# Kernel tuning notes

Hardware: AMD Instinct MI355X
Metric: run time of the kernel (lower is better)

## Reference

```python
import jax, jax.numpy as jnp
import numpy as np

N = 100000        # total nodes (60000 type-0 + 40000 type-1)
E = 1600000       # edges (avg degree 16)
D = 128           # num_hidden
C = 16            # num_classes


def _glorot(key, fan_in, fan_out):
    # xavier_normal with gain 1.414 (as in the torch module inits)
    std = 1.414 * (2.0 / (fan_in + fan_out)) ** 0.5
    return jax.random.normal(key, (fan_in, fan_out), jnp.float32) * std


def setup_inputs() -> dict:
    key = jax.random.key(0)
    ks = jax.random.split(key, 12)
    feat0 = jax.random.normal(ks[0], (60000, 512), jnp.float32)
    feat1 = jax.random.normal(ks[1], (40000, 256), jnp.float32)
    src = jax.random.randint(ks[2], (E,), 0, N, jnp.int32)
    dst = jax.random.randint(ks[3], (E,), 0, N, jnp.int32)
    return {
        "feat0": feat0,
        "feat1": feat1,
        "src": src,
        "dst": dst,
        "W_fc0": _glorot(ks[4], 512, D), "b_fc0": jnp.zeros((D,), jnp.float32),
        "W_fc1": _glorot(ks[5], 256, D), "b_fc1": jnp.zeros((D,), jnp.float32),
        "W_g0": _glorot(ks[6], D, D),   "b_g0": jnp.zeros((D,), jnp.float32),
        "W_g1": _glorot(ks[7], D, D),   "b_g1": jnp.zeros((D,), jnp.float32),
        "W_out": _glorot(ks[8], D, C),  "b_out": jnp.zeros((C,), jnp.float32),
    }


def reference(feat0, feat1, src, dst,
              W_fc0, b_fc0, W_fc1, b_fc1,
              W_g0, b_g0, W_g1, b_g1, W_out, b_out):
    # per-type input projections, then concat over node types -> (N, D)
    h = jnp.concatenate([feat0 @ W_fc0 + b_fc0, feat1 @ W_fc1 + b_fc1], axis=0)

    # in-degree for 'mean' reduce (DGL mean yields 0 for isolated nodes; clamp avoids /0)
    deg = jax.ops.segment_sum(jnp.ones((E,), jnp.float32), dst, num_segments=N)
    inv_deg = (1.0 / jnp.maximum(deg, 1.0))[:, None]

    def gin(h, W, b):
        # copy_u + mean reduce: neigh[i] = mean_{(j->i) in E} h[j]
        neigh = jax.ops.segment_sum(h[src], dst, num_segments=N) * inv_deg
        # (1 + eps) * h + neigh with eps = 0, then apply_func (Linear), then sigmoid
        return jax.nn.sigmoid((h + neigh) @ W + b)

    h = gin(h, W_g0, b_g0)      # gat_layers[0]
    h = gin(h, W_g1, b_g1)      # gat_layers[1]
    logits = gin(h, W_out, b_out)  # gat_layers[-1] -> (N, C)
    # logits.unsqueeze(1).mean(1) is a no-op
    return logits
```

## Files before the change

### kernel.cpp

```cpp
#include <hip/hip_runtime.h>
#include <hip/hip_bf16.h>

#define N_NODES 100000
#define N0_ROWS 60000
#define N1_ROWS 40000
#define NE 1600000
#define HD 128
#define NB 782
#define BSH 128
#define EPB 2560
#define NBLK 625

typedef __attribute__((ext_vector_type(8))) short short8;
typedef __attribute__((ext_vector_type(4))) float f32x4;

__device__ __forceinline__ float bf16lo(unsigned v) { return __uint_as_float(v << 16); }
__device__ __forceinline__ float bf16hi(unsigned v) { return __uint_as_float(v & 0xFFFF0000u); }

__device__ __forceinline__ unsigned short f2bf_rne(float f) {
    unsigned u = __float_as_uint(f);
    return (unsigned short)((u + 0x7FFFu + ((u >> 16) & 1u)) >> 16);
}
__device__ __forceinline__ unsigned pack2_rne(float lo, float hi) {
    unsigned a = __float_as_uint(lo); a = (a + 0x7FFFu + ((a >> 16) & 1u)) >> 16;
    unsigned b = __float_as_uint(hi); b = (b + 0x7FFFu + ((b >> 16) & 1u)) & 0xFFFF0000u;
    return (a & 0xFFFFu) | b;
}
__device__ __forceinline__ float sigmoidf_(float v) { return 1.0f / (1.0f + __expf(-v)); }

__global__ __launch_bounds__(256) void k_phist(const int* __restrict__ dst,
                                               int* __restrict__ cnt) {
    __shared__ int h[NB];
    int blk = blockIdx.x;
    for (int i = threadIdx.x; i < NB; i += 256) h[i] = 0;
    __syncthreads();
    int e0 = blk * EPB;
    for (int e = e0 + threadIdx.x; e < e0 + EPB; e += 256)
        atomicAdd(&h[dst[e] >> 7], 1);
    __syncthreads();
    for (int i = threadIdx.x; i < NB; i += 256)
        cnt[i * NBLK + blk] = h[i];
}

__global__ __launch_bounds__(64) void k_colscan(int* __restrict__ cnt,
                                                int* __restrict__ bcnt) {
    int b = blockIdx.x, lane = threadIdx.x & 63;
    int* col = cnt + (size_t)b * NBLK;
    int carry = 0;
    for (int base = 0; base < NBLK; base += 64) {
        int i = base + lane;
        int v = (i < NBLK) ? col[i] : 0;
        int s = v;
        #pragma unroll
        for (int off = 1; off < 64; off <<= 1) {
            int t = __shfl_up(s, off);
            if (lane >= off) s += t;
        }
        if (i < NBLK) col[i] = carry + s - v;
        carry += __shfl(s, 63);
    }
    if (lane == 0) bcnt[b] = carry;
}

__global__ void k_bscan(const int* __restrict__ bcnt, int* __restrict__ boff,
                        int* __restrict__ rowptr) {
    int lane = threadIdx.x & 63;
    const int CH = (NB + 63) / 64;
    int base = lane * CH;
    int t = 0;
    for (int c = 0; c < CH; ++c) {
        int i = base + c;
        t += (i < NB) ? bcnt[i] : 0;
    }
    int s = t;
    #pragma unroll
    for (int off = 1; off < 64; off <<= 1) {
        int u = __shfl_up(s, off);
        if (lane >= off) s += u;
    }
    int running = s - t;
    for (int c = 0; c < CH; ++c) {
        int i = base + c;
        if (i < NB) {
            boff[i] = running;
            running += bcnt[i];
        }
    }
    if (lane == 0) { boff[NB] = NE; rowptr[N_NODES] = NE; }
}

__global__ __launch_bounds__(256) void k_pplace(const int* __restrict__ src,
                                                const int* __restrict__ dst,
                                                const int* __restrict__ boff,
                                                const int* __restrict__ cnt,
                                                unsigned* __restrict__ ebuf) {
    __shared__ int h[NB];
    int blk = blockIdx.x;
    for (int i = threadIdx.x; i < NB; i += 256) h[i] = cnt[i * NBLK + blk];
    __syncthreads();
    int e0 = blk * EPB;
    for (int e = e0 + threadIdx.x; e < e0 + EPB; e += 256) {
        int d = dst[e];
        int b = d >> 7;
        int pos = atomicAdd(&h[b], 1);
        ebuf[boff[b] + pos] = ((unsigned)(d & 127) << 17) | (unsigned)src[e];
    }
}

__global__ __launch_bounds__(256) void k_bplace(const unsigned* __restrict__ ebuf,
                                                const int* __restrict__ boff,
                                                int* __restrict__ rowptr,
                                                float* __restrict__ invd,
                                                int* __restrict__ eidx) {
    __shared__ int cnt[BSH], off[BSH], lcnt[BSH];
    int b = blockIdx.x, tid = threadIdx.x;
    int e0 = boff[b], e1 = boff[b + 1];
    for (int i = tid; i < BSH; i += 256) { cnt[i] = 0; lcnt[i] = 0; }
    __syncthreads();
    for (int e = e0 + tid; e < e1; e += 256)
        atomicAdd(&cnt[ebuf[e] >> 17], 1);
    __syncthreads();
    if (tid < 64) {
        int lane = tid;
        int c0 = cnt[2 * lane], c1 = cnt[2 * lane + 1];
        int t = c0 + c1, s = t;
        #pragma unroll
        for (int o = 1; o < 64; o <<= 1) {
            int u = __shfl_up(s, o);
            if (lane >= o) s += u;
        }
        int excl = s - t;
        off[2 * lane] = excl;
        off[2 * lane + 1] = excl + c0;
    }
    __syncthreads();
    for (int i = tid; i < BSH; i += 256) {
        int node = b * BSH + i;
        if (node < N_NODES) {
            rowptr[node] = e0 + off[i];
            invd[node] = 1.0f / fmaxf((float)cnt[i], 1.0f);
        }
    }
    for (int e = e0 + tid; e < e1; e += 256) {
        unsigned ent = ebuf[e];
        int d = ent >> 17;
        int pos = e0 + off[d] + atomicAdd(&lcnt[d], 1);
        eidx[pos] = (int)(ent & 0x1FFFFu);
    }
}

__global__ void prep_w_all(const float* __restrict__ W0, unsigned short* __restrict__ T0,
                           const float* __restrict__ W1, unsigned short* __restrict__ T1,
                           const float* __restrict__ W2, unsigned short* __restrict__ T2,
                           const float* __restrict__ W3, unsigned short* __restrict__ T3,
                           const float* __restrict__ W4, unsigned short* __restrict__ T4) {
    int gid = blockIdx.x * blockDim.x + threadIdx.x;
    int stride = gridDim.x * blockDim.x;
    const int S0 = 512 * 128, S1 = 256 * 128, S2 = 128 * 128, S3 = 128 * 128, S4 = 128 * 16;
    const int E1 = S0 + S1, E2 = E1 + S2, E3 = E2 + S3, E4 = E3 + S4;
    for (int i = gid; i < E4; i += stride) {
        if (i < S0) {
            int n = i / 512, k = i - n * 512;
            T0[i] = f2bf_rne(W0[k * 128 + n]);
        } else if (i < E1) {
            int j = i - S0; int n = j / 256, k = j - n * 256;
            T1[j] = f2bf_rne(W1[k * 128 + n]);
        } else if (i < E2) {
            int j = i - E1; int n = j / 128, k = j - n * 128;
            T2[j] = f2bf_rne(W2[k * 128 + n]);
        } else if (i < E3) {
            int j = i - E2; int n = j / 128, k = j - n * 128;
            T3[j] = f2bf_rne(W3[k * 128 + n]);
        } else {
            int j = i - E3; int n = j / 128, k = j - n * 128;
            T4[j] = f2bf_rne(W4[k * 16 + n]);
        }
    }
}

template <int K>
__global__ __launch_bounds__(512, 4) void k_proj(const float* __restrict__ feat,
                                                 const unsigned short* __restrict__ Wt,
                                                 const float* __restrict__ bias,
                                                 unsigned short* __restrict__ hout,
                                                 int ntiles, int row_off) {
    constexpr int KC = K / 32;
    __shared__ unsigned short A_lds[16][K + 8];

    const int tid = threadIdx.x;
    const int lane = tid & 63, w = tid >> 6;
    const int g = lane >> 4, r16 = lane & 15;
    const int col = w * 16 + r16;

    short8 fb[KC];
    #pragma unroll
    for (int kc = 0; kc < KC; ++kc)
        fb[kc] = *reinterpret_cast<const short8*>(Wt + (size_t)col * K + kc * 32 + g * 8);
    const float bv = bias[col];

    const int srow = tid >> 5;
    const int sseg = tid & 31;

    for (int tile = blockIdx.x; tile < ntiles; tile += gridDim.x) {
        __syncthreads();
        const float4* rowp = reinterpret_cast<const float4*>(feat + (size_t)(tile * 16 + srow) * K);
        #pragma unroll
        for (int s = 0; s < K / 128; ++s) {
            float4 v = rowp[sseg + s * 32];
            unsigned lo = __builtin_amdgcn_perm(__float_as_uint(v.y), __float_as_uint(v.x), 0x07060302u);
            unsigned hi = __builtin_amdgcn_perm(__float_as_uint(v.w), __float_as_uint(v.z), 0x07060302u);
            *reinterpret_cast<uint2*>(&A_lds[srow][(sseg + s * 32) * 4]) = make_uint2(lo, hi);
        }
        __syncthreads();
        f32x4 acc = {0.f, 0.f, 0.f, 0.f};
        #pragma unroll
        for (int kc = 0; kc < KC; ++kc) {
            short8 fa = *reinterpret_cast<const short8*>(&A_lds[r16][kc * 32 + g * 8]);
            acc = __builtin_amdgcn_mfma_f32_16x16x32_bf16(fa, fb[kc], acc, 0, 0, 0);
        }
        #pragma unroll
        for (int r = 0; r < 4; ++r) {
            size_t orow = (size_t)(row_off + tile * 16 + g * 4 + r);
            hout[orow * HD + col] = f2bf_rne(acc[r] + bv);
        }
    }
}

__global__ __launch_bounds__(256, 4) void k_z_gemm(const unsigned short* __restrict__ x,
                                                   const unsigned short* __restrict__ Wt,
                                                   unsigned short* __restrict__ zout) {
    const int lane = threadIdx.x & 63, wid = threadIdx.x >> 6;
    const int g = lane >> 4, r16 = lane & 15;
    const int colbase = wid * 32;

    short8 fb[2][4];
    #pragma unroll
    for (int nt = 0; nt < 2; ++nt) {
        int n = colbase + nt * 16 + r16;
        #pragma unroll
        for (int kc = 0; kc < 4; ++kc)
            fb[nt][kc] = *reinterpret_cast<const short8*>(Wt + (size_t)n * HD + kc * 32 + g * 8);
    }

    const int ntiles = N_NODES / 16;
    for (int tile = blockIdx.x; tile < ntiles; tile += gridDim.x) {
        const unsigned short* ap = x + (size_t)(tile * 16 + r16) * HD;
        f32x4 acc0 = {0.f, 0.f, 0.f, 0.f};
        f32x4 acc1 = {0.f, 0.f, 0.f, 0.f};
        #pragma unroll
        for (int kc = 0; kc < 4; ++kc) {
            short8 fa = *reinterpret_cast<const short8*>(ap + kc * 32 + g * 8);
            acc0 = __builtin_amdgcn_mfma_f32_16x16x32_bf16(fa, fb[0][kc], acc0, 0, 0, 0);
            acc1 = __builtin_amdgcn_mfma_f32_16x16x32_bf16(fa, fb[1][kc], acc1, 0, 0, 0);
        }
        #pragma unroll
        for (int r = 0; r < 4; ++r) {
            size_t orow = (size_t)(tile * 16 + g * 4 + r);
            zout[orow * HD + colbase + r16]      = f2bf_rne(acc0[r]);
            zout[orow * HD + colbase + 16 + r16] = f2bf_rne(acc1[r]);
        }
    }
}

__global__ __launch_bounds__(256, 4) void k_aggz(const unsigned short* __restrict__ z,
                                                 const int* __restrict__ rowptr,
                                                 const int* __restrict__ eidx,
                                                 const float* __restrict__ invd,
                                                 const float* __restrict__ bias,
                                                 unsigned short* __restrict__ hout) {
    const unsigned* zp = reinterpret_cast<const unsigned*>(z);
    unsigned* hp = reinterpret_cast<unsigned*>(hout);
    int lane = threadIdx.x & 63, wid = threadIdx.x >> 6;
    float blo = bias[2 * lane], bhi = bias[2 * lane + 1];
    int nwaves = gridDim.x * 4;
    for (int node = blockIdx.x * 4 + wid; node < N_NODES; node += nwaves) {
        int rp0 = rowptr[node], rp1 = rowptr[node + 1];
        float a0 = 0.f, a1 = 0.f;
        for (int base = rp0; base < rp1; base += 64) {
            int m = rp1 - base; if (m > 64) m = 64;
            int idx = (lane < m) ? eidx[base + lane] : 0;
            int t = 0;
            for (; t + 4 <= m; t += 4) {
                int j0 = __shfl(idx, t), j1 = __shfl(idx, t + 1);
                int j2 = __shfl(idx, t + 2), j3 = __shfl(idx, t + 3);
                unsigned v0 = zp[(size_t)j0 * 64 + lane];
                unsigned v1 = zp[(size_t)j1 * 64 + lane];
                unsigned v2 = zp[(size_t)j2 * 64 + lane];
                unsigned v3 = zp[(size_t)j3 * 64 + lane];
                a0 += bf16lo(v0) + bf16lo(v1) + bf16lo(v2) + bf16lo(v3);
                a1 += bf16hi(v0) + bf16hi(v1) + bf16hi(v2) + bf16hi(v3);
            }
            for (; t < m; ++t) {
                int j = __shfl(idx, t);
                unsigned v = zp[(size_t)j * 64 + lane];
                a0 += bf16lo(v); a1 += bf16hi(v);
            }
        }
        unsigned zv = zp[(size_t)node * 64 + lane];
        float s = invd[node];
        hp[(size_t)node * 64 + lane] = pack2_rne(sigmoidf_(bf16lo(zv) + s * a0 + blo),
                                                 sigmoidf_(bf16hi(zv) + s * a1 + bhi));
    }
}

__global__ __launch_bounds__(256, 4) void k_zout_gemm(const unsigned short* __restrict__ x,
                                                      const unsigned short* __restrict__ Wt,
                                                      unsigned short* __restrict__ z3) {
    const int lane = threadIdx.x & 63, wid = threadIdx.x >> 6;
    const int g = lane >> 4, r16 = lane & 15;

    short8 fb[4];
    #pragma unroll
    for (int kc = 0; kc < 4; ++kc)
        fb[kc] = *reinterpret_cast<const short8*>(Wt + (size_t)r16 * HD + kc * 32 + g * 8);

    const int ntiles = N_NODES / 16;
    for (int tile = blockIdx.x * 4 + wid; tile < ntiles; tile += gridDim.x * 4) {
        const unsigned short* ap = x + (size_t)(tile * 16 + r16) * HD;
        f32x4 acc = {0.f, 0.f, 0.f, 0.f};
        #pragma unroll
        for (int kc = 0; kc < 4; ++kc) {
            short8 fa = *reinterpret_cast<const short8*>(ap + kc * 32 + g * 8);
            acc = __builtin_amdgcn_mfma_f32_16x16x32_bf16(fa, fb[kc], acc, 0, 0, 0);
        }
        #pragma unroll
        for (int r = 0; r < 4; ++r)
            z3[(size_t)(tile * 16 + g * 4 + r) * 16 + r16] = f2bf_rne(acc[r]);
    }
}

__global__ __launch_bounds__(256, 4) void k_agg16(const unsigned short* __restrict__ z3,
                                                  const int* __restrict__ rowptr,
                                                  const int* __restrict__ eidx,
                                                  const float* __restrict__ invd,
                                                  const float* __restrict__ bias,
                                                  float* __restrict__ out) {
    const unsigned* zp = reinterpret_cast<const unsigned*>(z3);
    int lane = threadIdx.x & 63, wid = threadIdx.x >> 6;
    int grp = lane >> 3, sub = lane & 7;
    float blo = bias[2 * sub], bhi = bias[2 * sub + 1];
    int step = gridDim.x * 32;
    for (int nb = blockIdx.x * 32 + wid * 8; nb < N_NODES; nb += step) {
        int node = nb + grp;
        bool valid = node < N_NODES;
        int rp0 = valid ? rowptr[node] : 0;
        int rp1 = valid ? rowptr[node + 1] : 0;
        float a0 = 0.f, a1 = 0.f;
        for (int base = rp0; base < rp1; base += 8) {
            int m = rp1 - base; if (m > 8) m = 8;
            int idx = (sub < m) ? eidx[base + sub] : 0;
            #pragma unroll
            for (int t = 0; t < 8; ++t) {
                if (t < m) {
                    int j = __shfl(idx, (grp << 3) + t);
                    unsigned v = zp[(size_t)j * 8 + sub];
                    a0 += bf16lo(v); a1 += bf16hi(v);
                }
            }
        }
        if (valid) {
            unsigned zv = zp[(size_t)node * 8 + sub];
            float s = invd[node];
            out[(size_t)node * 16 + sub * 2]     = sigmoidf_(bf16lo(zv) + s * a0 + blo);
            out[(size_t)node * 16 + sub * 2 + 1] = sigmoidf_(bf16hi(zv) + s * a1 + bhi);
        }
    }
}

extern "C" void kernel_launch(void* const* d_in, const int* in_sizes, int n_in,
                              void* d_out, int out_size, void* d_ws, size_t ws_size,
                              hipStream_t stream) {
    const float* feat0 = (const float*)d_in[0];
    const float* feat1 = (const float*)d_in[1];
    const int*   src   = (const int*)d_in[2];
    const int*   dst   = (const int*)d_in[3];
    const float* Wfc0  = (const float*)d_in[4];
    const float* bfc0  = (const float*)d_in[5];
    const float* Wfc1  = (const float*)d_in[6];
    const float* bfc1  = (const float*)d_in[7];
    const float* Wg0   = (const float*)d_in[8];
    const float* bg0   = (const float*)d_in[9];
    const float* Wg1   = (const float*)d_in[10];
    const float* bg1   = (const float*)d_in[11];
    const float* Wout  = (const float*)d_in[12];
    const float* bout  = (const float*)d_in[13];

    char* w = (char*)d_ws;
    auto alloc = [&](size_t bytes) {
        char* p = w;
        w += (bytes + 255) & ~(size_t)255;
        return p;
    };
    unsigned short* h      = (unsigned short*)alloc((size_t)N_NODES * HD * 2);
    unsigned short* z      = (unsigned short*)alloc((size_t)N_NODES * HD * 2);
    unsigned short* z3     = (unsigned short*)alloc((size_t)N_NODES * 16 * 2);
    int*   rowptr = (int*)alloc((size_t)(N_NODES + 1) * 4);
    float* invd   = (float*)alloc((size_t)N_NODES * 4);
    int*   eidx   = (int*)alloc((size_t)NE * 4);
    int*   cnt    = (int*)alloc((size_t)NB * NBLK * 4);
    int*   bcnt   = (int*)alloc((size_t)NB * 4);
    int*   boff   = (int*)alloc((size_t)(NB + 1) * 4);
    unsigned short* Wt_fc0 = (unsigned short*)alloc(512 * 128 * 2);
    unsigned short* Wt_fc1 = (unsigned short*)alloc(256 * 128 * 2);
    unsigned short* Wt_g0  = (unsigned short*)alloc(128 * 128 * 2);
    unsigned short* Wt_g1  = (unsigned short*)alloc(128 * 128 * 2);
    unsigned short* Wt_out = (unsigned short*)alloc(128 * 16 * 2);
    unsigned* ebuf = (unsigned*)z;

    k_phist<<<NBLK, 256, 0, stream>>>(dst, cnt);
    k_colscan<<<NB, 64, 0, stream>>>(cnt, bcnt);
    k_bscan<<<1, 64, 0, stream>>>(bcnt, boff, rowptr);
    k_pplace<<<NBLK, 256, 0, stream>>>(src, dst, boff, cnt, ebuf);
    k_bplace<<<NB, 256, 0, stream>>>(ebuf, boff, rowptr, invd, eidx);

    prep_w_all<<<520, 256, 0, stream>>>(Wfc0, Wt_fc0, Wfc1, Wt_fc1,
                                        Wg0, Wt_g0, Wg1, Wt_g1, Wout, Wt_out);

    k_proj<512><<<512, 512, 0, stream>>>(feat0, Wt_fc0, bfc0, h, N0_ROWS / 16, 0);
    k_proj<256><<<512, 512, 0, stream>>>(feat1, Wt_fc1, bfc1, h, N1_ROWS / 16, N0_ROWS);

    k_z_gemm<<<2084, 256, 0, stream>>>(h, Wt_g0, z);
    k_aggz<<<2048, 256, 0, stream>>>(z, rowptr, eidx, invd, bg0, h);
    k_z_gemm<<<2084, 256, 0, stream>>>(h, Wt_g1, z);
    k_aggz<<<2048, 256, 0, stream>>>(z, rowptr, eidx, invd, bg1, h);
    k_zout_gemm<<<1563, 256, 0, stream>>>(h, Wt_out, z3);
    k_agg16<<<2048, 256, 0, stream>>>(z3, rowptr, eidx, invd, bout, (float*)d_out);
}
```

Baseline: 304.0 us.

## Fuse dense GEMMs into projection and aggregation kernels via LDS tiles

The next layer's 128x128 GEMM now runs inside the input projection kernel, so z = h·W_g0 is produced directly from LDS and h never goes to global memory. Each GIN aggregation is fused with the following GEMM. A block gathers 16 nodes into an LDS tile and then runs the MFMA on that tile, which removes the separate z_gemm and zout_gemm launches and their h round-trips. In exchange, the aggregation is now tied to fixed 16-node tiles with block-wide barriers, so load imbalance across degrees can stall whole blocks, and the 16-class kernel uses only one wave for its MFMA. ebuf now gets its own buffer instead of aliasing z.

```diff
diff --git a/kernel.cpp b/kernel.cpp
--- a/kernel.cpp
+++ b/kernel.cpp
@@ -179,13 +179,15 @@
 }
 
 template <int K>
-__global__ __launch_bounds__(512, 4) void k_proj(const float* __restrict__ feat,
-                                                 const unsigned short* __restrict__ Wt,
-                                                 const float* __restrict__ bias,
-                                                 unsigned short* __restrict__ hout,
-                                                 int ntiles, int row_off) {
+__global__ __launch_bounds__(512, 4) void k_proj_fused(const float* __restrict__ feat,
+                                                       const unsigned short* __restrict__ Wt,
+                                                       const float* __restrict__ bias,
+                                                       const unsigned short* __restrict__ Wg,
+                                                       unsigned short* __restrict__ zout,
+                                                       int ntiles, int row_off) {
     constexpr int KC = K / 32;
     __shared__ unsigned short A_lds[16][K + 8];
+    __shared__ unsigned short h_lds[16][HD + 8];
 
     const int tid = threadIdx.x;
     const int lane = tid & 63, w = tid >> 6;
@@ -196,6 +198,10 @@
     #pragma unroll
     for (int kc = 0; kc < KC; ++kc)
         fb[kc] = *reinterpret_cast<const short8*>(Wt + (size_t)col * K + kc * 32 + g * 8);
+    short8 fbg[4];
+    #pragma unroll
+    for (int kc = 0; kc < 4; ++kc)
+        fbg[kc] = *reinterpret_cast<const short8*>(Wg + (size_t)col * HD + kc * 32 + g * 8);
     const float bv = bias[col];
 
     const int srow = tid >> 5;
@@ -219,16 +225,32 @@
             acc = __builtin_amdgcn_mfma_f32_16x16x32_bf16(fa, fb[kc], acc, 0, 0, 0);
         }
         #pragma unroll
+        for (int r = 0; r < 4; ++r)
+            h_lds[g * 4 + r][col] = f2bf_rne(acc[r] + bv);
+        __syncthreads();
+        f32x4 accz = {0.f, 0.f, 0.f, 0.f};
+        #pragma unroll
+        for (int kc = 0; kc < 4; ++kc) {
+            short8 fa = *reinterpret_cast<const short8*>(&h_lds[r16][kc * 32 + g * 8]);
+            accz = __builtin_amdgcn_mfma_f32_16x16x32_bf16(fa, fbg[kc], accz, 0, 0, 0);
+        }
+        #pragma unroll
         for (int r = 0; r < 4; ++r) {
             size_t orow = (size_t)(row_off + tile * 16 + g * 4 + r);
-            hout[orow * HD + col] = f2bf_rne(acc[r] + bv);
-        }
-    }
-}
-
-__global__ __launch_bounds__(256, 4) void k_z_gemm(const unsigned short* __restrict__ x,
-                                                   const unsigned short* __restrict__ Wt,
-                                                   unsigned short* __restrict__ zout) {
+            zout[orow * HD + col] = f2bf_rne(accz[r]);
+        }
+    }
+}
+
+__global__ __launch_bounds__(256, 4) void k_agg_gemm128(const unsigned short* __restrict__ z,
+                                                        const int* __restrict__ rowptr,
+                                                        const int* __restrict__ eidx,
+                                                        const float* __restrict__ invd,
+                                                        const float* __restrict__ bias,
+                                                        const unsigned short* __restrict__ Wt,
+                                                        unsigned short* __restrict__ zout) {
+    __shared__ unsigned short h_lds[16][HD + 8];
+    const unsigned* zp = reinterpret_cast<const unsigned*>(z);
     const int lane = threadIdx.x & 63, wid = threadIdx.x >> 6;
     const int g = lane >> 4, r16 = lane & 15;
     const int colbase = wid * 32;
@@ -241,15 +263,48 @@
         for (int kc = 0; kc < 4; ++kc)
             fb[nt][kc] = *reinterpret_cast<const short8*>(Wt + (size_t)n * HD + kc * 32 + g * 8);
     }
+    const float blo = bias[2 * lane], bhi = bias[2 * lane + 1];
 
     const int ntiles = N_NODES / 16;
     for (int tile = blockIdx.x; tile < ntiles; tile += gridDim.x) {
-        const unsigned short* ap = x + (size_t)(tile * 16 + r16) * HD;
+        __syncthreads();
+        #pragma unroll
+        for (int q = 0; q < 4; ++q) {
+            int node = tile * 16 + wid * 4 + q;
+            int rp0 = rowptr[node], rp1 = rowptr[node + 1];
+            float a0 = 0.f, a1 = 0.f;
+            for (int base = rp0; base < rp1; base += 64) {
+                int m = rp1 - base; if (m > 64) m = 64;
+                int idx = (lane < m) ? eidx[base + lane] : 0;
+                int t = 0;
+                for (; t + 4 <= m; t += 4) {
+                    int j0 = __shfl(idx, t), j1 = __shfl(idx, t + 1);
+                    int j2 = __shfl(idx, t + 2), j3 = __shfl(idx, t + 3);
+                    unsigned v0 = zp[(size_t)j0 * 64 + lane];
+                    unsigned v1 = zp[(size_t)j1 * 64 + lane];
+                    unsigned v2 = zp[(size_t)j2 * 64 + lane];
+                    unsigned v3 = zp[(size_t)j3 * 64 + lane];
+                    a0 += bf16lo(v0) + bf16lo(v1) + bf16lo(v2) + bf16lo(v3);
+                    a1 += bf16hi(v0) + bf16hi(v1) + bf16hi(v2) + bf16hi(v3);
+                }
+                for (; t < m; ++t) {
+                    int j = __shfl(idx, t);
+                    unsigned v = zp[(size_t)j * 64 + lane];
+                    a0 += bf16lo(v); a1 += bf16hi(v);
+                }
+            }
+            unsigned zv = zp[(size_t)node * 64 + lane];
+            float s = invd[node];
+            *reinterpret_cast<unsigned*>(&h_lds[wid * 4 + q][2 * lane]) =
+                pack2_rne(sigmoidf_(bf16lo(zv) + s * a0 + blo),
+                          sigmoidf_(bf16hi(zv) + s * a1 + bhi));
+        }
+        __syncthreads();
         f32x4 acc0 = {0.f, 0.f, 0.f, 0.f};
         f32x4 acc1 = {0.f, 0.f, 0.f, 0.f};
         #pragma unroll
         for (int kc = 0; kc < 4; ++kc) {
-            short8 fa = *reinterpret_cast<const short8*>(ap + kc * 32 + g * 8);
+            short8 fa = *reinterpret_cast<const short8*>(&h_lds[r16][kc * 32 + g * 8]);
             acc0 = __builtin_amdgcn_mfma_f32_16x16x32_bf16(fa, fb[0][kc], acc0, 0, 0, 0);
             acc1 = __builtin_amdgcn_mfma_f32_16x16x32_bf16(fa, fb[1][kc], acc1, 0, 0, 0);
         }
@@ -262,50 +317,15 @@
     }
 }
 
-__global__ __launch_bounds__(256, 4) void k_aggz(const unsigned short* __restrict__ z,
-                                                 const int* __restrict__ rowptr,
-                                                 const int* __restrict__ eidx,
-                                                 const float* __restrict__ invd,
-                                                 const float* __restrict__ bias,
-                                                 unsigned short* __restrict__ hout) {
+__global__ __launch_bounds__(256, 4) void k_agg_gemm16(const unsigned short* __restrict__ z,
+                                                       const int* __restrict__ rowptr,
+                                                       const int* __restrict__ eidx,
+                                                       const float* __restrict__ invd,
+                                                       const float* __restrict__ bias,
+                                                       const unsigned short* __restrict__ Wt,
+                                                       unsigned short* __restrict__ z3) {
+    __shared__ unsigned short h_lds[16][HD + 8];
     const unsigned* zp = reinterpret_cast<const unsigned*>(z);
-    unsigned* hp = reinterpret_cast<unsigned*>(hout);
-    int lane = threadIdx.x & 63, wid = threadIdx.x >> 6;
-    float blo = bias[2 * lane], bhi = bias[2 * lane + 1];
-    int nwaves = gridDim.x * 4;
-    for (int node = blockIdx.x * 4 + wid; node < N_NODES; node += nwaves) {
-        int rp0 = rowptr[node], rp1 = rowptr[node + 1];
-        float a0 = 0.f, a1 = 0.f;
-        for (int base = rp0; base < rp1; base += 64) {
-            int m = rp1 - base; if (m > 64) m = 64;
-            int idx = (lane < m) ? eidx[base + lane] : 0;
-            int t = 0;
-            for (; t + 4 <= m; t += 4) {
-                int j0 = __shfl(idx, t), j1 = __shfl(idx, t + 1);
-                int j2 = __shfl(idx, t + 2), j3 = __shfl(idx, t + 3);
-                unsigned v0 = zp[(size_t)j0 * 64 + lane];
-                unsigned v1 = zp[(size_t)j1 * 64 + lane];
-                unsigned v2 = zp[(size_t)j2 * 64 + lane];
-                unsigned v3 = zp[(size_t)j3 * 64 + lane];
-                a0 += bf16lo(v0) + bf16lo(v1) + bf16lo(v2) + bf16lo(v3);
-                a1 += bf16hi(v0) + bf16hi(v1) + bf16hi(v2) + bf16hi(v3);
-            }
-            for (; t < m; ++t) {
-                int j = __shfl(idx, t);
-                unsigned v = zp[(size_t)j * 64 + lane];
-                a0 += bf16lo(v); a1 += bf16hi(v);
-            }
-        }
-        unsigned zv = zp[(size_t)node * 64 + lane];
-        float s = invd[node];
-        hp[(size_t)node * 64 + lane] = pack2_rne(sigmoidf_(bf16lo(zv) + s * a0 + blo),
-                                                 sigmoidf_(bf16hi(zv) + s * a1 + bhi));
-    }
-}
-
-__global__ __launch_bounds__(256, 4) void k_zout_gemm(const unsigned short* __restrict__ x,
-                                                      const unsigned short* __restrict__ Wt,
-                                                      unsigned short* __restrict__ z3) {
     const int lane = threadIdx.x & 63, wid = threadIdx.x >> 6;
     const int g = lane >> 4, r16 = lane & 15;
 
@@ -313,19 +333,54 @@
     #pragma unroll
     for (int kc = 0; kc < 4; ++kc)
         fb[kc] = *reinterpret_cast<const short8*>(Wt + (size_t)r16 * HD + kc * 32 + g * 8);
+    const float blo = bias[2 * lane], bhi = bias[2 * lane + 1];
 
     const int ntiles = N_NODES / 16;
-    for (int tile = blockIdx.x * 4 + wid; tile < ntiles; tile += gridDim.x * 4) {
-        const unsigned short* ap = x + (size_t)(tile * 16 + r16) * HD;
-        f32x4 acc = {0.f, 0.f, 0.f, 0.f};
-        #pragma unroll
-        for (int kc = 0; kc < 4; ++kc) {
-            short8 fa = *reinterpret_cast<const short8*>(ap + kc * 32 + g * 8);
-            acc = __builtin_amdgcn_mfma_f32_16x16x32_bf16(fa, fb[kc], acc, 0, 0, 0);
-        }
-        #pragma unroll
-        for (int r = 0; r < 4; ++r)
-            z3[(size_t)(tile * 16 + g * 4 + r) * 16 + r16] = f2bf_rne(acc[r]);
+    for (int tile = blockIdx.x; tile < ntiles; tile += gridDim.x) {
+        __syncthreads();
+        #pragma unroll
+        for (int q = 0; q < 4; ++q) {
+            int node = tile * 16 + wid * 4 + q;
+            int rp0 = rowptr[node], rp1 = rowptr[node + 1];
+            float a0 = 0.f, a1 = 0.f;
+            for (int base = rp0; base < rp1; base += 64) {
+                int m = rp1 - base; if (m > 64) m = 64;
+                int idx = (lane < m) ? eidx[base + lane] : 0;
+                int t = 0;
+                for (; t + 4 <= m; t += 4) {
+                    int j0 = __shfl(idx, t), j1 = __shfl(idx, t + 1);
+                    int j2 = __shfl(idx, t + 2), j3 = __shfl(idx, t + 3);
+                    unsigned v0 = zp[(size_t)j0 * 64 + lane];
+                    unsigned v1 = zp[(size_t)j1 * 64 + lane];
+                    unsigned v2 = zp[(size_t)j2 * 64 + lane];
+                    unsigned v3 = zp[(size_t)j3 * 64 + lane];
+                    a0 += bf16lo(v0) + bf16lo(v1) + bf16lo(v2) + bf16lo(v3);
+                    a1 += bf16hi(v0) + bf16hi(v1) + bf16hi(v2) + bf16hi(v3);
+                }
+                for (; t < m; ++t) {
+                    int j = __shfl(idx, t);
+                    unsigned v = zp[(size_t)j * 64 + lane];
+                    a0 += bf16lo(v); a1 += bf16hi(v);
+                }
+            }
+            unsigned zv = zp[(size_t)node * 64 + lane];
+            float s = invd[node];
+            *reinterpret_cast<unsigned*>(&h_lds[wid * 4 + q][2 * lane]) =
+                pack2_rne(sigmoidf_(bf16lo(zv) + s * a0 + blo),
+                          sigmoidf_(bf16hi(zv) + s * a1 + bhi));
+        }
+        __syncthreads();
+        if (wid == 0) {
+            f32x4 acc = {0.f, 0.f, 0.f, 0.f};
+            #pragma unroll
+            for (int kc = 0; kc < 4; ++kc) {
+                short8 fa = *reinterpret_cast<const short8*>(&h_lds[r16][kc * 32 + g * 8]);
+                acc = __builtin_amdgcn_mfma_f32_16x16x32_bf16(fa, fb[kc], acc, 0, 0, 0);
+            }
+            #pragma unroll
+            for (int r = 0; r < 4; ++r)
+                z3[(size_t)(tile * 16 + g * 4 + r) * 16 + r16] = f2bf_rne(acc[r]);
+        }
     }
 }
 
@@ -391,12 +446,13 @@
         w += (bytes + 255) & ~(size_t)255;
         return p;
     };
-    unsigned short* h      = (unsigned short*)alloc((size_t)N_NODES * HD * 2);
-    unsigned short* z      = (unsigned short*)alloc((size_t)N_NODES * HD * 2);
+    unsigned short* zA     = (unsigned short*)alloc((size_t)N_NODES * HD * 2);
+    unsigned short* zB     = (unsigned short*)alloc((size_t)N_NODES * HD * 2);
     unsigned short* z3     = (unsigned short*)alloc((size_t)N_NODES * 16 * 2);
     int*   rowptr = (int*)alloc((size_t)(N_NODES + 1) * 4);
     float* invd   = (float*)alloc((size_t)N_NODES * 4);
     int*   eidx   = (int*)alloc((size_t)NE * 4);
+    unsigned* ebuf = (unsigned*)alloc((size_t)NE * 4);
     int*   cnt    = (int*)alloc((size_t)NB * NBLK * 4);
     int*   bcnt   = (int*)alloc((size_t)NB * 4);
     int*   boff   = (int*)alloc((size_t)(NB + 1) * 4);
@@ -405,7 +461,6 @@
     unsigned short* Wt_g0  = (unsigned short*)alloc(128 * 128 * 2);
     unsigned short* Wt_g1  = (unsigned short*)alloc(128 * 128 * 2);
     unsigned short* Wt_out = (unsigned short*)alloc(128 * 16 * 2);
-    unsigned* ebuf = (unsigned*)z;
 
     k_phist<<<NBLK, 256, 0, stream>>>(dst, cnt);
     k_colscan<<<NB, 64, 0, stream>>>(cnt, bcnt);
@@ -416,13 +471,10 @@
     prep_w_all<<<520, 256, 0, stream>>>(Wfc0, Wt_fc0, Wfc1, Wt_fc1,
                                         Wg0, Wt_g0, Wg1, Wt_g1, Wout, Wt_out);
 
-    k_proj<512><<<512, 512, 0, stream>>>(feat0, Wt_fc0, bfc0, h, N0_ROWS / 16, 0);
-    k_proj<256><<<512, 512, 0, stream>>>(feat1, Wt_fc1, bfc1, h, N1_ROWS / 16, N0_ROWS);
-
-    k_z_gemm<<<2084, 256, 0, stream>>>(h, Wt_g0, z);
-    k_aggz<<<2048, 256, 0, stream>>>(z, rowptr, eidx, invd, bg0, h);
-    k_z_gemm<<<2084, 256, 0, stream>>>(h, Wt_g1, z);
-    k_aggz<<<2048, 256, 0, stream>>>(z, rowptr, eidx, invd, bg1, h);
-    k_zout_gemm<<<1563, 256, 0, stream>>>(h, Wt_out, z3);
+    k_proj_fused<512><<<512, 512, 0, stream>>>(feat0, Wt_fc0, bfc0, Wt_g0, zA, N0_ROWS / 16, 0);
+    k_proj_fused<256><<<512, 512, 0, stream>>>(feat1, Wt_fc1, bfc1, Wt_g0, zA, N1_ROWS / 16, N0_ROWS);
+
+    k_agg_gemm128<<<2084, 256, 0, stream>>>(zA, rowptr, eidx, invd, bg0, Wt_g1, zB);
+    k_agg_gemm16<<<2084, 256, 0, stream>>>(zB, rowptr, eidx, invd, bg1, Wt_out, z3);
     k_agg16<<<2048, 256, 0, stream>>>(z3, rowptr, eidx, invd, bout, (float*)d_out);
 }
```

Result: slower. 319.1 us (+5.0%).

## Gather neighbours from an FP8 copy of z and fuse projection with first GEMM

Applied to the files above, without the earlier changes.

The input-projection kernel now also runs the first GIN weight GEMM from LDS, so the h tensor is never written out and read back before layer 0. The z GEMMs additionally emit an FP8 (e4m3) packed copy of z. The mean-aggregation kernels gather neighbour rows from that FP8 copy, halving the bytes moved by the random per-edge loads, while keeping the bf16 z for the self term. This trades numerical accuracy in the neighbour sum for reduced gather bandwidth. It also adds extra LDS round trips and barriers in the GEMM kernels, plus a separate edge buffer allocation.

```diff
diff --git a/kernel.cpp b/kernel.cpp
--- a/kernel.cpp
+++ b/kernel.cpp
@@ -13,6 +13,7 @@
 
 typedef __attribute__((ext_vector_type(8))) short short8;
 typedef __attribute__((ext_vector_type(4))) float f32x4;
+typedef __attribute__((ext_vector_type(2))) float f32x2;
 
 __device__ __forceinline__ float bf16lo(unsigned v) { return __uint_as_float(v << 16); }
 __device__ __forceinline__ float bf16hi(unsigned v) { return __uint_as_float(v & 0xFFFF0000u); }
@@ -27,6 +28,56 @@
     return (a & 0xFFFFu) | b;
 }
 __device__ __forceinline__ float sigmoidf_(float v) { return 1.0f / (1.0f + __expf(-v)); }
+
+#if defined(__has_builtin)
+#if __has_builtin(__builtin_amdgcn_cvt_pk_fp8_f32) && __has_builtin(__builtin_amdgcn_cvt_pk_f32_fp8)
+#define HAS_FP8_CVT 1
+#endif
+#endif
+
+#ifdef HAS_FP8_CVT
+__device__ __forceinline__ unsigned pack4_fp8(float c0, float c1, float c2, float c3) {
+    int r = 0;
+    r = __builtin_amdgcn_cvt_pk_fp8_f32(c0, c1, r, false);
+    r = __builtin_amdgcn_cvt_pk_fp8_f32(c2, c3, r, true);
+    return (unsigned)r;
+}
+__device__ __forceinline__ f32x2 unpack2_fp8(unsigned u16) {
+    return __builtin_amdgcn_cvt_pk_f32_fp8((int)u16, false);
+}
+#else
+__device__ __forceinline__ unsigned enc1_fp8(float f) {
+    f = fminf(448.f, fmaxf(-448.f, f));
+    float a = fabsf(f);
+    unsigned s = (__float_as_uint(f) >> 31) << 7;
+    if (a >= 0.015625f) {
+        unsigned u = __float_as_uint(a);
+        u += 0x7FFFFu + ((u >> 20) & 1u);
+        int E = (int)((u >> 23) & 255) - 120;
+        unsigned m3 = (u >> 20) & 7;
+        if (E > 15) { E = 15; m3 = 6; }
+        return s | ((unsigned)E << 3) | m3;
+    } else {
+        int q = (int)rintf(a * 512.f);
+        if (q >= 8) return s | (1u << 3);
+        return s | (unsigned)q;
+    }
+}
+__device__ __forceinline__ unsigned pack4_fp8(float c0, float c1, float c2, float c3) {
+    return enc1_fp8(c0) | (enc1_fp8(c1) << 8) | (enc1_fp8(c2) << 16) | (enc1_fp8(c3) << 24);
+}
+__device__ __forceinline__ float dec1_fp8(unsigned b) {
+    unsigned s = (b >> 7) & 1, e = (b >> 3) & 15, m = b & 7;
+    float v = e ? ldexpf((float)(8 + m), (int)e - 10) : ldexpf((float)m, -9);
+    return s ? -v : v;
+}
+__device__ __forceinline__ f32x2 unpack2_fp8(unsigned u16) {
+    f32x2 r;
+    r[0] = dec1_fp8(u16 & 0xFFu);
+    r[1] = dec1_fp8((u16 >> 8) & 0xFFu);
+    return r;
+}
+#endif
 
 __global__ __launch_bounds__(256) void k_phist(const int* __restrict__ dst,
                                                int* __restrict__ cnt) {
@@ -179,13 +230,16 @@
 }
 
 template <int K>
-__global__ __launch_bounds__(512, 4) void k_proj(const float* __restrict__ feat,
-                                                 const unsigned short* __restrict__ Wt,
-                                                 const float* __restrict__ bias,
-                                                 unsigned short* __restrict__ hout,
-                                                 int ntiles, int row_off) {
+__global__ __launch_bounds__(512, 4) void k_proj_fused(const float* __restrict__ feat,
+                                                       const unsigned short* __restrict__ Wt,
+                                                       const float* __restrict__ bias,
+                                                       const unsigned short* __restrict__ Wg,
+                                                       unsigned short* __restrict__ zout,
+                                                       unsigned* __restrict__ z8out,
+                                                       int ntiles, int row_off) {
     constexpr int KC = K / 32;
     __shared__ unsigned short A_lds[16][K + 8];
+    __shared__ unsigned short h_lds[16][HD + 8];
 
     const int tid = threadIdx.x;
     const int lane = tid & 63, w = tid >> 6;
@@ -196,6 +250,10 @@
     #pragma unroll
     for (int kc = 0; kc < KC; ++kc)
         fb[kc] = *reinterpret_cast<const short8*>(Wt + (size_t)col * K + kc * 32 + g * 8);
+    short8 fbg[4];
+    #pragma unroll
+    for (int kc = 0; kc < 4; ++kc)
+        fbg[kc] = *reinterpret_cast<const short8*>(Wg + (size_t)col * HD + kc * 32 + g * 8);
     const float bv = bias[col];
 
     const int srow = tid >> 5;
@@ -219,19 +277,47 @@
             acc = __builtin_amdgcn_mfma_f32_16x16x32_bf16(fa, fb[kc], acc, 0, 0, 0);
         }
         #pragma unroll
+        for (int r = 0; r < 4; ++r)
+            h_lds[g * 4 + r][col] = f2bf_rne(acc[r] + bv);
+        __syncthreads();
+        f32x4 accz = {0.f, 0.f, 0.f, 0.f};
+        #pragma unroll
+        for (int kc = 0; kc < 4; ++kc) {
+            short8 fa = *reinterpret_cast<const short8*>(&h_lds[r16][kc * 32 + g * 8]);
+            accz = __builtin_amdgcn_mfma_f32_16x16x32_bf16(fa, fbg[kc], accz, 0, 0, 0);
+        }
+        #pragma unroll
         for (int r = 0; r < 4; ++r) {
             size_t orow = (size_t)(row_off + tile * 16 + g * 4 + r);
-            hout[orow * HD + col] = f2bf_rne(acc[r] + bv);
+            zout[orow * HD + col] = f2bf_rne(accz[r]);
+        }
+        __syncthreads();
+        #pragma unroll
+        for (int r = 0; r < 4; ++r)
+            h_lds[g * 4 + r][col] = f2bf_rne(accz[r]);
+        __syncthreads();
+        {
+            int c4 = sseg * 4;
+            unsigned p = pack4_fp8(
+                bf16lo((unsigned)h_lds[srow][c4])     ,
+                bf16lo((unsigned)h_lds[srow][c4 + 1]) ,
+                bf16lo((unsigned)h_lds[srow][c4 + 2]) ,
+                bf16lo((unsigned)h_lds[srow][c4 + 3]) );
+            z8out[(size_t)(row_off + tile * 16 + srow) * 32 + sseg] = p;
         }
     }
 }
 
 __global__ __launch_bounds__(256, 4) void k_z_gemm(const unsigned short* __restrict__ x,
                                                    const unsigned short* __restrict__ Wt,
-                                                   unsigned short* __restrict__ zout) {
+                                                   unsigned short* __restrict__ zout,
+                                                   unsigned* __restrict__ z8out) {
+    __shared__ unsigned short h_lds[16][HD + 8];
     const int lane = threadIdx.x & 63, wid = threadIdx.x >> 6;
     const int g = lane >> 4, r16 = lane & 15;
     const int colbase = wid * 32;
+    const int prow = threadIdx.x >> 4;
+    const int pseg = threadIdx.x & 15;
 
     short8 fb[2][4];
     #pragma unroll
@@ -253,21 +339,43 @@
             acc0 = __builtin_amdgcn_mfma_f32_16x16x32_bf16(fa, fb[0][kc], acc0, 0, 0, 0);
             acc1 = __builtin_amdgcn_mfma_f32_16x16x32_bf16(fa, fb[1][kc], acc1, 0, 0, 0);
         }
+        __syncthreads();
         #pragma unroll
         for (int r = 0; r < 4; ++r) {
             size_t orow = (size_t)(tile * 16 + g * 4 + r);
-            zout[orow * HD + colbase + r16]      = f2bf_rne(acc0[r]);
-            zout[orow * HD + colbase + 16 + r16] = f2bf_rne(acc1[r]);
-        }
-    }
-}
-
-__global__ __launch_bounds__(256, 4) void k_aggz(const unsigned short* __restrict__ z,
-                                                 const int* __restrict__ rowptr,
-                                                 const int* __restrict__ eidx,
-                                                 const float* __restrict__ invd,
-                                                 const float* __restrict__ bias,
-                                                 unsigned short* __restrict__ hout) {
+            unsigned short zb0 = f2bf_rne(acc0[r]);
+            unsigned short zb1 = f2bf_rne(acc1[r]);
+            zout[orow * HD + colbase + r16]      = zb0;
+            zout[orow * HD + colbase + 16 + r16] = zb1;
+            h_lds[g * 4 + r][colbase + r16]      = zb0;
+            h_lds[g * 4 + r][colbase + 16 + r16] = zb1;
+        }
+        __syncthreads();
+        {
+            int c8 = pseg * 8;
+            unsigned p0 = pack4_fp8(
+                bf16lo((unsigned)h_lds[prow][c8])     ,
+                bf16lo((unsigned)h_lds[prow][c8 + 1]) ,
+                bf16lo((unsigned)h_lds[prow][c8 + 2]) ,
+                bf16lo((unsigned)h_lds[prow][c8 + 3]) );
+            unsigned p1 = pack4_fp8(
+                bf16lo((unsigned)h_lds[prow][c8 + 4]) ,
+                bf16lo((unsigned)h_lds[prow][c8 + 5]) ,
+                bf16lo((unsigned)h_lds[prow][c8 + 6]) ,
+                bf16lo((unsigned)h_lds[prow][c8 + 7]) );
+            *reinterpret_cast<uint2*>(&z8out[(size_t)(tile * 16 + prow) * 32 + pseg * 2]) =
+                make_uint2(p0, p1);
+        }
+    }
+}
+
+__global__ __launch_bounds__(256, 4) void k_aggz8(const unsigned short* __restrict__ z,
+                                                  const unsigned short* __restrict__ z8,
+                                                  const int* __restrict__ rowptr,
+                                                  const int* __restrict__ eidx,
+                                                  const float* __restrict__ invd,
+                                                  const float* __restrict__ bias,
+                                                  unsigned short* __restrict__ hout) {
     const unsigned* zp = reinterpret_cast<const unsigned*>(z);
     unsigned* hp = reinterpret_cast<unsigned*>(hout);
     int lane = threadIdx.x & 63, wid = threadIdx.x >> 6;
@@ -275,7 +383,7 @@
     int nwaves = gridDim.x * 4;
     for (int node = blockIdx.x * 4 + wid; node < N_NODES; node += nwaves) {
         int rp0 = rowptr[node], rp1 = rowptr[node + 1];
-        float a0 = 0.f, a1 = 0.f;
+        float a0 = 0.f, a1 = 0.f, b0 = 0.f, b1 = 0.f;
         for (int base = rp0; base < rp1; base += 64) {
             int m = rp1 - base; if (m > 64) m = 64;
             int idx = (lane < m) ? eidx[base + lane] : 0;
@@ -283,19 +391,22 @@
             for (; t + 4 <= m; t += 4) {
                 int j0 = __shfl(idx, t), j1 = __shfl(idx, t + 1);
                 int j2 = __shfl(idx, t + 2), j3 = __shfl(idx, t + 3);
-                unsigned v0 = zp[(size_t)j0 * 64 + lane];
-                unsigned v1 = zp[(size_t)j1 * 64 + lane];
-                unsigned v2 = zp[(size_t)j2 * 64 + lane];
-                unsigned v3 = zp[(size_t)j3 * 64 + lane];
-                a0 += bf16lo(v0) + bf16lo(v1) + bf16lo(v2) + bf16lo(v3);
-                a1 += bf16hi(v0) + bf16hi(v1) + bf16hi(v2) + bf16hi(v3);
+                unsigned u0 = z8[(size_t)j0 * 64 + lane];
+                unsigned u1 = z8[(size_t)j1 * 64 + lane];
+                unsigned u2 = z8[(size_t)j2 * 64 + lane];
+                unsigned u3 = z8[(size_t)j3 * 64 + lane];
+                f32x2 d0 = unpack2_fp8(u0), d1 = unpack2_fp8(u1);
+                f32x2 d2 = unpack2_fp8(u2), d3 = unpack2_fp8(u3);
+                a0 += d0[0] + d1[0]; a1 += d0[1] + d1[1];
+                b0 += d2[0] + d3[0]; b1 += d2[1] + d3[1];
             }
             for (; t < m; ++t) {
                 int j = __shfl(idx, t);
-                unsigned v = zp[(size_t)j * 64 + lane];
-                a0 += bf16lo(v); a1 += bf16hi(v);
+                f32x2 d = unpack2_fp8(z8[(size_t)j * 64 + lane]);
+                a0 += d[0]; a1 += d[1];
             }
         }
+        a0 += b0; a1 += b1;
         unsigned zv = zp[(size_t)node * 64 + lane];
         float s = invd[node];
         hp[(size_t)node * 64 + lane] = pack2_rne(sigmoidf_(bf16lo(zv) + s * a0 + blo),
@@ -391,12 +502,16 @@
         w += (bytes + 255) & ~(size_t)255;
         return p;
     };
-    unsigned short* h      = (unsigned short*)alloc((size_t)N_NODES * HD * 2);
-    unsigned short* z      = (unsigned short*)alloc((size_t)N_NODES * HD * 2);
-    unsigned short* z3     = (unsigned short*)alloc((size_t)N_NODES * 16 * 2);
+    unsigned short* zA  = (unsigned short*)alloc((size_t)N_NODES * HD * 2);
+    unsigned short* zB  = (unsigned short*)alloc((size_t)N_NODES * HD * 2);
+    unsigned short* h   = (unsigned short*)alloc((size_t)N_NODES * HD * 2);
+    unsigned* z8A = (unsigned*)alloc((size_t)N_NODES * HD);
+    unsigned* z8B = (unsigned*)alloc((size_t)N_NODES * HD);
+    unsigned short* z3  = (unsigned short*)alloc((size_t)N_NODES * 16 * 2);
     int*   rowptr = (int*)alloc((size_t)(N_NODES + 1) * 4);
     float* invd   = (float*)alloc((size_t)N_NODES * 4);
     int*   eidx   = (int*)alloc((size_t)NE * 4);
+    unsigned* ebuf = (unsigned*)alloc((size_t)NE * 4);
     int*   cnt    = (int*)alloc((size_t)NB * NBLK * 4);
     int*   bcnt   = (int*)alloc((size_t)NB * 4);
     int*   boff   = (int*)alloc((size_t)(NB + 1) * 4);
@@ -405,7 +520,6 @@
     unsigned short* Wt_g0  = (unsigned short*)alloc(128 * 128 * 2);
     unsigned short* Wt_g1  = (unsigned short*)alloc(128 * 128 * 2);
     unsigned short* Wt_out = (unsigned short*)alloc(128 * 16 * 2);
-    unsigned* ebuf = (unsigned*)z;
 
     k_phist<<<NBLK, 256, 0, stream>>>(dst, cnt);
     k_colscan<<<NB, 64, 0, stream>>>(cnt, bcnt);
@@ -416,13 +530,12 @@
     prep_w_all<<<520, 256, 0, stream>>>(Wfc0, Wt_fc0, Wfc1, Wt_fc1,
                                         Wg0, Wt_g0, Wg1, Wt_g1, Wout, Wt_out);
 
-    k_proj<512><<<512, 512, 0, stream>>>(feat0, Wt_fc0, bfc0, h, N0_ROWS / 16, 0);
-    k_proj<256><<<512, 512, 0, stream>>>(feat1, Wt_fc1, bfc1, h, N1_ROWS / 16, N0_ROWS);
-
-    k_z_gemm<<<2084, 256, 0, stream>>>(h, Wt_g0, z);
-    k_aggz<<<2048, 256, 0, stream>>>(z, rowptr, eidx, invd, bg0, h);
-    k_z_gemm<<<2084, 256, 0, stream>>>(h, Wt_g1, z);
-    k_aggz<<<2048, 256, 0, stream>>>(z, rowptr, eidx, invd, bg1, h);
+    k_proj_fused<512><<<512, 512, 0, stream>>>(feat0, Wt_fc0, bfc0, Wt_g0, zA, z8A, N0_ROWS / 16, 0);
+    k_proj_fused<256><<<512, 512, 0, stream>>>(feat1, Wt_fc1, bfc1, Wt_g0, zA, z8A, N1_ROWS / 16, N0_ROWS);
+
+    k_aggz8<<<2048, 256, 0, stream>>>(zA, (const unsigned short*)z8A, rowptr, eidx, invd, bg0, h);
+    k_z_gemm<<<2084, 256, 0, stream>>>(h, Wt_g1, zB, z8B);
+    k_aggz8<<<2048, 256, 0, stream>>>(zB, (const unsigned short*)z8B, rowptr, eidx, invd, bg1, h);
     k_zout_gemm<<<1563, 256, 0, stream>>>(h, Wt_out, z3);
     k_agg16<<<2048, 256, 0, stream>>>(z3, rowptr, eidx, invd, bout, (float*)d_out);
 }
```

New measurement: 277.1 us. -8.9%, faster.
